# Kernel tuning notes

Hardware: AMD Instinct MI355X
Metric: run time of the kernel (lower is better)

Reference implementation:

```python
import jax, jax.numpy as jnp
import numpy as np

B, S, D, H = 2, 2048, 1024, 16
DH = D // H


def setup_inputs() -> dict:
    key = jax.random.key(0)
    ks = jax.random.split(key, 6)
    scale = 1.0 / np.sqrt(D)
    x = jax.random.normal(ks[0], (B, S, D), dtype=jnp.float32)
    mask = jnp.tril(jnp.ones((S, S), dtype=jnp.int32))  # causal 0/1 mask
    Wq = jax.random.normal(ks[1], (D, D), dtype=jnp.float32) * scale
    Wk = jax.random.normal(ks[2], (D, D), dtype=jnp.float32) * scale
    Wv = jax.random.normal(ks[3], (D, D), dtype=jnp.float32) * scale
    Wo = jax.random.normal(ks[4], (D, D), dtype=jnp.float32) * scale
    z = jnp.zeros((D,), dtype=jnp.float32)
    return {"x": x, "mask": mask, "Wq": Wq, "bq": z, "Wk": Wk, "bk": z,
            "Wv": Wv, "bv": z, "Wo": Wo, "bo": z}


def reference(x, mask, Wq, bq, Wk, bk, Wv, bv, Wo, bo):
    # Linear projections (torch Linear: x @ W.T + b; here W stored as [in, out])
    Q = x @ Wq + bq
    K = x @ Wk + bk
    V = x @ Wv + bv
    # [B, S, D] -> [B, H, S, DH]
    Q = Q.reshape(B, S, H, DH).transpose(0, 2, 1, 3)
    K = K.reshape(B, S, H, DH).transpose(0, 2, 1, 3)
    V = V.reshape(B, S, H, DH).transpose(0, 2, 1, 3)
    # scores: [B, H, S, S]
    attn = jnp.einsum('bhqd,bhkd->bhqk', Q, K) / jnp.sqrt(jnp.float32(DH))
    attn = jnp.where(mask == 0, jnp.float32(-1e9), attn)
    scores = jax.nn.softmax(attn, axis=-1)
    # dropout is identity in eval mode
    out = jnp.einsum('bhqk,bhkd->bhqd', scores, V)
    out = out.transpose(0, 2, 1, 3).reshape(B, S, D)
    return out @ Wo + bo
```

## Files before the change

kernel.cpp:

```cpp
#include <hip/hip_runtime.h>
#include <hip/hip_bf16.h>


typedef short bf16x8 __attribute__((ext_vector_type(8)));
typedef float f32x4  __attribute__((ext_vector_type(4)));
typedef short s16x4  __attribute__((ext_vector_type(4)));

#define BB 2
#define SS 2048
#define DD 1024
#define HH 16
#define DHH 64

__device__ __forceinline__ unsigned short f2bf(float f) {
    unsigned u = __builtin_bit_cast(unsigned, f);
    u += 0x7FFFu + ((u >> 16) & 1u);
    return (unsigned short)(u >> 16);
}
__device__ __forceinline__ unsigned short f2bf_trunc(float f) {
    return (unsigned short)(__builtin_bit_cast(unsigned, f) >> 16);
}
__device__ __forceinline__ void cp16(const unsigned short* g, unsigned short* l) {
    __builtin_amdgcn_global_load_lds(
        (const __attribute__((address_space(1))) unsigned int*)(g),
        (__attribute__((address_space(3))) unsigned int*)(l), 16, 0, 0);
}

__global__ __launch_bounds__(256) void prep(
    const float* __restrict__ x,
    const float* __restrict__ w0, const float* __restrict__ w1,
    const float* __restrict__ w2, const float* __restrict__ w3,
    unsigned short* __restrict__ xbf, unsigned short* __restrict__ wt) {
    __shared__ float tile[64][65];
    const int bid = blockIdx.x;
    const int tid = threadIdx.x;
    if (bid < 4096) {
        int i = (bid * 256 + tid) * 4;
        float4 v = *reinterpret_cast<const float4*>(x + i);
        s16x4 p;
        p[0] = (short)f2bf(v.x); p[1] = (short)f2bf(v.y);
        p[2] = (short)f2bf(v.z); p[3] = (short)f2bf(v.w);
        *reinterpret_cast<s16x4*>(xbf + i) = p;
        return;
    }
    const int tb = bid - 4096;
    const int z  = tb >> 8;
    const int bx = (tb & 15) * 64, by = ((tb >> 4) & 15) * 64;
    const float* src = z == 0 ? w0 : z == 1 ? w1 : z == 2 ? w2 : w3;
    unsigned short* out = wt + (size_t)z * (DD * DD);
    const int tx = tid & 63, ty = tid >> 6;
    #pragma unroll
    for (int i = 0; i < 64; i += 4)
        tile[ty + i][tx] = src[(size_t)(by + ty + i) * DD + bx + tx];
    __syncthreads();
    #pragma unroll
    for (int i = 0; i < 64; i += 4)
        out[(size_t)(bx + ty + i) * DD + by + tx] = f2bf(tile[tx][ty + i]);
}

__global__ __launch_bounds__(256) void gemm_qkv(
    const unsigned short* __restrict__ A, const unsigned short* __restrict__ Wt,
    const float* __restrict__ b0, const float* __restrict__ b1,
    const float* __restrict__ b2,
    unsigned short* __restrict__ d0, unsigned short* __restrict__ d1,
    unsigned short* __restrict__ d2) {
    __shared__ __align__(16) unsigned short As[128 * 64];
    __shared__ __align__(16) unsigned short Bs[128 * 64];

    const int tid  = threadIdx.x;
    const int lane = tid & 63;
    const int w    = tid >> 6;
    const int col  = lane & 15;
    const int quad = lane >> 4;
    const int wm   = (w >> 1) * 64;
    const int wn   = (w & 1) * 64;
    const int mb   = blockIdx.y * 128;
    const int nb   = blockIdx.x * 128;

    const int r8 = lane >> 3, gg = lane & 7;
    const int srcoff = ((gg ^ r8) * 8);
    const int cswz = col & 7;

    f32x4 acc[4][4];
    #pragma unroll
    for (int i = 0; i < 4; i++)
        #pragma unroll
        for (int j = 0; j < 4; j++) acc[i][j] = (f32x4){0.f, 0.f, 0.f, 0.f};

    for (int kt = 0; kt < 1024; kt += 64) {
        __syncthreads();
        #pragma unroll
        for (int it = 0; it < 4; it++) {
            int row = w * 32 + it * 8 + r8;
            cp16(A  + (size_t)(mb + row) * 1024 + kt + srcoff, As + (w * 32 + it * 8) * 64);
            cp16(Wt + (size_t)(nb + row) * 1024 + kt + srcoff, Bs + (w * 32 + it * 8) * 64);
        }
        __syncthreads();
        #pragma unroll
        for (int kk = 0; kk < 64; kk += 32) {
            const int kg = (kk >> 3) + quad;
            const int pos = ((kg ^ cswz) * 8);
            bf16x8 af[4], bfr[4];
            #pragma unroll
            for (int i = 0; i < 4; i++)
                af[i] = *reinterpret_cast<const bf16x8*>(As + (wm + i * 16 + col) * 64 + pos);
            #pragma unroll
            for (int j = 0; j < 4; j++)
                bfr[j] = *reinterpret_cast<const bf16x8*>(Bs + (wn + j * 16 + col) * 64 + pos);
            #pragma unroll
            for (int i = 0; i < 4; i++)
                #pragma unroll
                for (int j = 0; j < 4; j++)
                    acc[i][j] = __builtin_amdgcn_mfma_f32_16x16x32_bf16(af[i], bfr[j], acc[i][j], 0, 0, 0);
        }
    }

    const float QSCALE = 0.125f * 1.44269504f;
    #pragma unroll
    for (int i = 0; i < 4; i++) {
        int mg = mb + wm + i * 16 + quad * 4;
        #pragma unroll
        for (int j = 0; j < 4; j++) {
            int ng = nb + wn + j * 16 + col;
            int sel = ng >> 10, n2 = ng & 1023;
            int h = n2 >> 6, dd2 = n2 & 63;
            int b = mg >> 11, s = mg & 2047;
            int bh = b * HH + h;
            const float* bp = sel == 0 ? b0 : sel == 1 ? b1 : b2;
            float bbv = bp[n2];
            if (sel == 0) {
                #pragma unroll
                for (int r = 0; r < 4; r++)
                    d0[((size_t)bh * SS + s + r) * DHH + dd2] = f2bf((acc[i][j][r] + bbv) * QSCALE);
            } else if (sel == 1) {
                #pragma unroll
                for (int r = 0; r < 4; r++)
                    d1[((size_t)bh * SS + s + r) * DHH + dd2] = f2bf(acc[i][j][r] + bbv);
            } else {
                s16x4 pack;
                #pragma unroll
                for (int r = 0; r < 4; r++) pack[r] = (short)f2bf(acc[i][j][r] + bbv);
                *reinterpret_cast<s16x4*>(d2 + ((size_t)bh * DHH + dd2) * SS + s) = pack;
            }
        }
    }
}

__global__ __launch_bounds__(256) void gemm_out(
    const unsigned short* __restrict__ A, const unsigned short* __restrict__ Wt,
    const float* __restrict__ b0, float* __restrict__ d0f) {
    __shared__ __align__(16) unsigned short As[128 * 64];
    __shared__ __align__(16) unsigned short Bs[64 * 64];

    const int tid  = threadIdx.x;
    const int lane = tid & 63;
    const int w    = tid >> 6;
    const int col  = lane & 15;
    const int quad = lane >> 4;
    const int wm   = (w >> 1) * 64;
    const int wn   = (w & 1) * 32;
    const int mb   = blockIdx.y * 128;
    const int nb   = blockIdx.x * 64;

    const int r8 = lane >> 3, gg = lane & 7;
    const int srcoff = ((gg ^ r8) * 8);
    const int cswz = col & 7;

    f32x4 acc[4][2];
    #pragma unroll
    for (int i = 0; i < 4; i++)
        #pragma unroll
        for (int j = 0; j < 2; j++) acc[i][j] = (f32x4){0.f, 0.f, 0.f, 0.f};

    for (int kt = 0; kt < 1024; kt += 64) {
        __syncthreads();
        #pragma unroll
        for (int it = 0; it < 4; it++) {
            int row = w * 32 + it * 8 + r8;
            cp16(A + (size_t)(mb + row) * 1024 + kt + srcoff, As + (w * 32 + it * 8) * 64);
        }
        cp16(Wt + (size_t)(nb + w * 16 + r8) * 1024 + kt + srcoff, Bs + (w * 16) * 64);
        cp16(Wt + (size_t)(nb + w * 16 + 8 + r8) * 1024 + kt + srcoff, Bs + (w * 16 + 8) * 64);
        __syncthreads();
        #pragma unroll
        for (int kk = 0; kk < 64; kk += 32) {
            const int kg = (kk >> 3) + quad;
            const int pos = ((kg ^ cswz) * 8);
            bf16x8 af[4], bfr[2];
            #pragma unroll
            for (int i = 0; i < 4; i++)
                af[i] = *reinterpret_cast<const bf16x8*>(As + (wm + i * 16 + col) * 64 + pos);
            #pragma unroll
            for (int j = 0; j < 2; j++)
                bfr[j] = *reinterpret_cast<const bf16x8*>(Bs + (wn + j * 16 + col) * 64 + pos);
            #pragma unroll
            for (int i = 0; i < 4; i++)
                #pragma unroll
                for (int j = 0; j < 2; j++)
                    acc[i][j] = __builtin_amdgcn_mfma_f32_16x16x32_bf16(af[i], bfr[j], acc[i][j], 0, 0, 0);
        }
    }

    #pragma unroll
    for (int i = 0; i < 4; i++) {
        int mg = mb + wm + i * 16 + quad * 4;
        #pragma unroll
        for (int j = 0; j < 2; j++) {
            int ng = nb + wn + j * 16 + col;
            float bbv = b0[ng];
            #pragma unroll
            for (int r = 0; r < 4; r++)
                d0f[(size_t)(mg + r) * 1024 + ng] = acc[i][j][r] + bbv;
        }
    }
}

__global__ __launch_bounds__(256, 3) void attn(
    const unsigned short* __restrict__ Q, const unsigned short* __restrict__ K,
    const unsigned short* __restrict__ Vt, unsigned short* __restrict__ O) {
    __shared__ __align__(16) unsigned short Ks[2][64 * 64];
    __shared__ __align__(16) unsigned short Vs[2][64 * 64];
    __shared__ __align__(16) unsigned short Ps[4][16 * 72];

    const int tid  = threadIdx.x;
    const int lane = tid & 63;
    const int w    = tid >> 6;
    const int col  = lane & 15;
    const int quad = lane >> 4;
    const int bh   = blockIdx.x & 31;
    const int qt   = 31 - (blockIdx.x >> 5);
    const int qb   = qt * 64;
    const int r8 = lane >> 3, gg = lane & 7;
    const int srcoff = ((gg ^ r8) * 8);
    const int cswz = col & 7;
    const int pos0 = (quad       ^ cswz) * 8;
    const int pos1 = ((4 + quad) ^ cswz) * 8;

    bf16x8 onesf;
    #pragma unroll
    for (int j = 0; j < 8; j++) onesf[j] = (col == 0) ? (short)0x3F80 : (short)0;

    const int qrow = qb + w * 16 + col;
    const size_t qbase = ((size_t)bh * SS + qrow) * DHH;
    bf16x8 qlo = *reinterpret_cast<const bf16x8*>(Q + qbase + quad * 8);
    bf16x8 qhi = *reinterpret_cast<const bf16x8*>(Q + qbase + 32 + quad * 8);

    f32x4 o[5];
    #pragma unroll
    for (int d = 0; d < 5; d++) o[d] = (f32x4){0.f, 0.f, 0.f, 0.f};
    float m_i[4];
    #pragma unroll
    for (int r = 0; r < 4; r++) m_i[r] = -1e30f;

    const int ntiles = qt + 1;
    for (int t0 = 0; t0 < ntiles; t0 += 2) {
        const bool two = (t0 + 1 < ntiles);
        __syncthreads();
        #pragma unroll
        for (int it = 0; it < 2; it++) {
            int row = w * 16 + it * 8 + r8;
            cp16(K  + ((size_t)bh * SS + t0 * 64 + row) * DHH + srcoff,
                 Ks[0] + (w * 16 + it * 8) * 64);
            cp16(Vt + ((size_t)bh * DHH + row) * SS + t0 * 64 + srcoff,
                 Vs[0] + (w * 16 + it * 8) * 64);
        }
        if (two) {
            #pragma unroll
            for (int it = 0; it < 2; it++) {
                int row = w * 16 + it * 8 + r8;
                cp16(K  + ((size_t)bh * SS + (t0 + 1) * 64 + row) * DHH + srcoff,
                     Ks[1] + (w * 16 + it * 8) * 64);
                cp16(Vt + ((size_t)bh * DHH + row) * SS + (t0 + 1) * 64 + srcoff,
                     Vs[1] + (w * 16 + it * 8) * 64);
            }
        }
        __syncthreads();

        f32x4 sc[8];
        #pragma unroll
        for (int nt = 0; nt < 4; nt++) {
            int key = nt * 16 + col;
            bf16x8 klo = *reinterpret_cast<const bf16x8*>(Ks[0] + key * 64 + pos0);
            bf16x8 khi = *reinterpret_cast<const bf16x8*>(Ks[0] + key * 64 + pos1);
            f32x4 z = (f32x4){0.f, 0.f, 0.f, 0.f};
            z = __builtin_amdgcn_mfma_f32_16x16x32_bf16(qlo, klo, z, 0, 0, 0);
            z = __builtin_amdgcn_mfma_f32_16x16x32_bf16(qhi, khi, z, 0, 0, 0);
            sc[nt] = z;
        }
        if (two) {
            #pragma unroll
            for (int nt = 0; nt < 4; nt++) {
                int key = nt * 16 + col;
                bf16x8 klo = *reinterpret_cast<const bf16x8*>(Ks[1] + key * 64 + pos0);
                bf16x8 khi = *reinterpret_cast<const bf16x8*>(Ks[1] + key * 64 + pos1);
                f32x4 z = (f32x4){0.f, 0.f, 0.f, 0.f};
                z = __builtin_amdgcn_mfma_f32_16x16x32_bf16(qlo, klo, z, 0, 0, 0);
                z = __builtin_amdgcn_mfma_f32_16x16x32_bf16(qhi, khi, z, 0, 0, 0);
                sc[4 + nt] = z;
            }
        }
        if (t0 == qt || (two && t0 + 1 == qt)) {
            const int sb = (t0 == qt) ? 0 : 4;
            const int tb = (t0 == qt) ? t0 : t0 + 1;
            #pragma unroll
            for (int nt = 0; nt < 4; nt++) {
                int kg = tb * 64 + nt * 16 + col;
                #pragma unroll
                for (int r = 0; r < 4; r++) {
                    int qg = qb + w * 16 + quad * 4 + r;
                    if (kg > qg) sc[sb + nt][r] = -3.0e38f;
                }
            }
        }
        float mnew[4];
        bool upd = false;
        #pragma unroll
        for (int r = 0; r < 4; r++) {
            float t = fmaxf(fmaxf(sc[0][r], sc[1][r]), fmaxf(sc[2][r], sc[3][r]));
            if (two)
                t = fmaxf(t, fmaxf(fmaxf(sc[4][r], sc[5][r]), fmaxf(sc[6][r], sc[7][r])));
            t = fmaxf(t, __shfl_xor(t, 1));
            t = fmaxf(t, __shfl_xor(t, 2));
            t = fmaxf(t, __shfl_xor(t, 4));
            t = fmaxf(t, __shfl_xor(t, 8));
            mnew[r] = fmaxf(m_i[r], t);
            upd = upd || (mnew[r] > m_i[r]);
        }
        if (__any(upd)) {
            #pragma unroll
            for (int r = 0; r < 4; r++) {
                float a = exp2f(m_i[r] - mnew[r]);
                #pragma unroll
                for (int d = 0; d < 5; d++) o[d][r] *= a;
            }
        }
        #pragma unroll
        for (int r = 0; r < 4; r++) m_i[r] = mnew[r];

        unsigned short* pw = Ps[w];
        #pragma unroll
        for (int nt = 0; nt < 4; nt++)
            #pragma unroll
            for (int r = 0; r < 4; r++)
                pw[(quad * 4 + r) * 72 + nt * 16 + col] = f2bf_trunc(exp2f(sc[nt][r] - mnew[r]));
        {
            bf16x8 pf0 = *reinterpret_cast<const bf16x8*>(pw + col * 72 + quad * 8);
            bf16x8 pf1 = *reinterpret_cast<const bf16x8*>(pw + col * 72 + 32 + quad * 8);
            #pragma unroll
            for (int dt = 0; dt < 4; dt++) {
                int rv = dt * 16 + col;
                bf16x8 vf0 = *reinterpret_cast<const bf16x8*>(Vs[0] + rv * 64 + pos0);
                bf16x8 vf1 = *reinterpret_cast<const bf16x8*>(Vs[0] + rv * 64 + pos1);
                o[dt] = __builtin_amdgcn_mfma_f32_16x16x32_bf16(pf0, vf0, o[dt], 0, 0, 0);
                o[dt] = __builtin_amdgcn_mfma_f32_16x16x32_bf16(pf1, vf1, o[dt], 0, 0, 0);
            }
            o[4] = __builtin_amdgcn_mfma_f32_16x16x32_bf16(pf0, onesf, o[4], 0, 0, 0);
            o[4] = __builtin_amdgcn_mfma_f32_16x16x32_bf16(pf1, onesf, o[4], 0, 0, 0);
        }
        if (two) {
            #pragma unroll
            for (int nt = 0; nt < 4; nt++)
                #pragma unroll
                for (int r = 0; r < 4; r++)
                    pw[(quad * 4 + r) * 72 + nt * 16 + col] = f2bf_trunc(exp2f(sc[4 + nt][r] - mnew[r]));
            bf16x8 pf0 = *reinterpret_cast<const bf16x8*>(pw + col * 72 + quad * 8);
            bf16x8 pf1 = *reinterpret_cast<const bf16x8*>(pw + col * 72 + 32 + quad * 8);
            #pragma unroll
            for (int dt = 0; dt < 4; dt++) {
                int rv = dt * 16 + col;
                bf16x8 vf0 = *reinterpret_cast<const bf16x8*>(Vs[1] + rv * 64 + pos0);
                bf16x8 vf1 = *reinterpret_cast<const bf16x8*>(Vs[1] + rv * 64 + pos1);
                o[dt] = __builtin_amdgcn_mfma_f32_16x16x32_bf16(pf0, vf0, o[dt], 0, 0, 0);
                o[dt] = __builtin_amdgcn_mfma_f32_16x16x32_bf16(pf1, vf1, o[dt], 0, 0, 0);
            }
            o[4] = __builtin_amdgcn_mfma_f32_16x16x32_bf16(pf0, onesf, o[4], 0, 0, 0);
            o[4] = __builtin_amdgcn_mfma_f32_16x16x32_bf16(pf1, onesf, o[4], 0, 0, 0);
        }
    }

    #pragma unroll
    for (int r = 0; r < 4; r++) {
        float lv = __shfl(o[4][r], lane & 48);
        float inv = 1.0f / lv;
        int sq = qb + w * 16 + quad * 4 + r;
        size_t base = ((size_t)(bh >> 4) * SS + sq) * DD + (size_t)(bh & 15) * DHH;
        #pragma unroll
        for (int dt = 0; dt < 4; dt++)
            O[base + dt * 16 + col] = f2bf(o[dt][r] * inv);
    }
}

extern "C" void kernel_launch(void* const* d_in, const int* in_sizes, int n_in,
                              void* d_out, int out_size, void* d_ws, size_t ws_size,
                              hipStream_t stream) {
    (void)in_sizes; (void)n_in; (void)out_size; (void)ws_size;
    const float* x  = (const float*)d_in[0];
    const float* Wq = (const float*)d_in[2];
    const float* bq = (const float*)d_in[3];
    const float* Wk = (const float*)d_in[4];
    const float* bk = (const float*)d_in[5];
    const float* Wv = (const float*)d_in[6];
    const float* bv = (const float*)d_in[7];
    const float* Wo = (const float*)d_in[8];
    const float* bo = (const float*)d_in[9];
    float* out = (float*)d_out;

    char* ws = (char*)d_ws;
    unsigned short* xbf = (unsigned short*)(ws);
    unsigned short* qws = (unsigned short*)(ws + ((size_t)8  << 20));
    unsigned short* kws = (unsigned short*)(ws + ((size_t)16 << 20));
    unsigned short* vws = (unsigned short*)(ws + ((size_t)24 << 20));
    unsigned short* wt  = (unsigned short*)(ws + ((size_t)32 << 20));
    unsigned short* ows = xbf;

    prep<<<dim3(5120), 256, 0, stream>>>(x, Wq, Wk, Wv, Wo, xbf, wt);
    gemm_qkv<<<dim3(24, 32), 256, 0, stream>>>(xbf, wt, bq, bk, bv,
                                               qws, kws, vws);
    attn<<<dim3(1024), 256, 0, stream>>>(qws, kws, vws, ows);
    gemm_out<<<dim3(16, 32), 256, 0, stream>>>(ows, wt + (size_t)3 * 1024 * 1024,
                                               bo, out);
}
```

Before: 211.5 us.

## Compute transposed scores so P stays in registers, dropping LDS round-trip

The QK^T MFMA operands are swapped so each lane holds scores for a single query row across keys. K rows are loaded into LDS in a permuted order so the register layout of the probabilities matches the A-operand layout the PV MFMA expects. This removes the per-wave P staging buffer in shared memory and its store/load round-trip. The row max now needs only two cross-lane shuffles, and the rescale factor is fetched per row with a shuffle. Launch bounds are raised to 5 blocks per CU to use the freed LDS and registers, at the risk of register pressure or spills.

```diff
diff --git a/kernel.cpp b/kernel.cpp
--- a/kernel.cpp
+++ b/kernel.cpp
@@ -215,12 +215,11 @@
     }
 }
 
-__global__ __launch_bounds__(256, 3) void attn(
+__global__ __launch_bounds__(256, 5) void attn(
     const unsigned short* __restrict__ Q, const unsigned short* __restrict__ K,
     const unsigned short* __restrict__ Vt, unsigned short* __restrict__ O) {
     __shared__ __align__(16) unsigned short Ks[2][64 * 64];
     __shared__ __align__(16) unsigned short Vs[2][64 * 64];
-    __shared__ __align__(16) unsigned short Ps[4][16 * 72];
 
     const int tid  = threadIdx.x;
     const int lane = tid & 63;
@@ -248,9 +247,7 @@
     f32x4 o[5];
     #pragma unroll
     for (int d = 0; d < 5; d++) o[d] = (f32x4){0.f, 0.f, 0.f, 0.f};
-    float m_i[4];
-    #pragma unroll
-    for (int r = 0; r < 4; r++) m_i[r] = -1e30f;
+    float m_i = -1e30f;
 
     const int ntiles = qt + 1;
     for (int t0 = 0; t0 < ntiles; t0 += 2) {
@@ -258,20 +255,22 @@
         __syncthreads();
         #pragma unroll
         for (int it = 0; it < 2; it++) {
-            int row = w * 16 + it * 8 + r8;
-            cp16(K  + ((size_t)bh * SS + t0 * 64 + row) * DHH + srcoff,
-                 Ks[0] + (w * 16 + it * 8) * 64);
-            cp16(Vt + ((size_t)bh * DHH + row) * SS + t0 * 64 + srcoff,
-                 Vs[0] + (w * 16 + it * 8) * 64);
+            int drow = w * 16 + it * 8;
+            int skey = (w >> 1) * 32 + it * 16 + (r8 >> 2) * 8 + (w & 1) * 4 + (r8 & 3);
+            cp16(K  + ((size_t)bh * SS + t0 * 64 + skey) * DHH + srcoff,
+                 Ks[0] + drow * 64);
+            cp16(Vt + ((size_t)bh * DHH + drow + r8) * SS + t0 * 64 + srcoff,
+                 Vs[0] + drow * 64);
         }
         if (two) {
             #pragma unroll
             for (int it = 0; it < 2; it++) {
-                int row = w * 16 + it * 8 + r8;
-                cp16(K  + ((size_t)bh * SS + (t0 + 1) * 64 + row) * DHH + srcoff,
-                     Ks[1] + (w * 16 + it * 8) * 64);
-                cp16(Vt + ((size_t)bh * DHH + row) * SS + (t0 + 1) * 64 + srcoff,
-                     Vs[1] + (w * 16 + it * 8) * 64);
+                int drow = w * 16 + it * 8;
+                int skey = (w >> 1) * 32 + it * 16 + (r8 >> 2) * 8 + (w & 1) * 4 + (r8 & 3);
+                cp16(K  + ((size_t)bh * SS + (t0 + 1) * 64 + skey) * DHH + srcoff,
+                     Ks[1] + drow * 64);
+                cp16(Vt + ((size_t)bh * DHH + drow + r8) * SS + (t0 + 1) * 64 + srcoff,
+                     Vs[1] + drow * 64);
             }
         }
         __syncthreads();
@@ -279,23 +278,23 @@
         f32x4 sc[8];
         #pragma unroll
         for (int nt = 0; nt < 4; nt++) {
-            int key = nt * 16 + col;
-            bf16x8 klo = *reinterpret_cast<const bf16x8*>(Ks[0] + key * 64 + pos0);
-            bf16x8 khi = *reinterpret_cast<const bf16x8*>(Ks[0] + key * 64 + pos1);
+            int krow = nt * 16 + col;
+            bf16x8 klo = *reinterpret_cast<const bf16x8*>(Ks[0] + krow * 64 + pos0);
+            bf16x8 khi = *reinterpret_cast<const bf16x8*>(Ks[0] + krow * 64 + pos1);
             f32x4 z = (f32x4){0.f, 0.f, 0.f, 0.f};
-            z = __builtin_amdgcn_mfma_f32_16x16x32_bf16(qlo, klo, z, 0, 0, 0);
-            z = __builtin_amdgcn_mfma_f32_16x16x32_bf16(qhi, khi, z, 0, 0, 0);
+            z = __builtin_amdgcn_mfma_f32_16x16x32_bf16(klo, qlo, z, 0, 0, 0);
+            z = __builtin_amdgcn_mfma_f32_16x16x32_bf16(khi, qhi, z, 0, 0, 0);
             sc[nt] = z;
         }
         if (two) {
             #pragma unroll
             for (int nt = 0; nt < 4; nt++) {
-                int key = nt * 16 + col;
-                bf16x8 klo = *reinterpret_cast<const bf16x8*>(Ks[1] + key * 64 + pos0);
-                bf16x8 khi = *reinterpret_cast<const bf16x8*>(Ks[1] + key * 64 + pos1);
+                int krow = nt * 16 + col;
+                bf16x8 klo = *reinterpret_cast<const bf16x8*>(Ks[1] + krow * 64 + pos0);
+                bf16x8 khi = *reinterpret_cast<const bf16x8*>(Ks[1] + krow * 64 + pos1);
                 f32x4 z = (f32x4){0.f, 0.f, 0.f, 0.f};
-                z = __builtin_amdgcn_mfma_f32_16x16x32_bf16(qlo, klo, z, 0, 0, 0);
-                z = __builtin_amdgcn_mfma_f32_16x16x32_bf16(qhi, khi, z, 0, 0, 0);
+                z = __builtin_amdgcn_mfma_f32_16x16x32_bf16(klo, qlo, z, 0, 0, 0);
+                z = __builtin_amdgcn_mfma_f32_16x16x32_bf16(khi, qhi, z, 0, 0, 0);
                 sc[4 + nt] = z;
             }
         }
@@ -304,48 +303,44 @@
             const int tb = (t0 == qt) ? t0 : t0 + 1;
             #pragma unroll
             for (int nt = 0; nt < 4; nt++) {
-                int kg = tb * 64 + nt * 16 + col;
                 #pragma unroll
                 for (int r = 0; r < 4; r++) {
-                    int qg = qb + w * 16 + quad * 4 + r;
-                    if (kg > qg) sc[sb + nt][r] = -3.0e38f;
+                    int kg = tb * 64 + (nt >> 1) * 32 + quad * 8 + (nt & 1) * 4 + r;
+                    if (kg > qrow) sc[sb + nt][r] = -3.0e38f;
                 }
             }
         }
-        float mnew[4];
-        bool upd = false;
-        #pragma unroll
-        for (int r = 0; r < 4; r++) {
-            float t = fmaxf(fmaxf(sc[0][r], sc[1][r]), fmaxf(sc[2][r], sc[3][r]));
-            if (two)
-                t = fmaxf(t, fmaxf(fmaxf(sc[4][r], sc[5][r]), fmaxf(sc[6][r], sc[7][r])));
-            t = fmaxf(t, __shfl_xor(t, 1));
-            t = fmaxf(t, __shfl_xor(t, 2));
-            t = fmaxf(t, __shfl_xor(t, 4));
-            t = fmaxf(t, __shfl_xor(t, 8));
-            mnew[r] = fmaxf(m_i[r], t);
-            upd = upd || (mnew[r] > m_i[r]);
-        }
+        float mx = fmaxf(fmaxf(sc[0][0], sc[0][1]), fmaxf(sc[0][2], sc[0][3]));
+        #pragma unroll
+        for (int nt = 1; nt < 4; nt++)
+            mx = fmaxf(mx, fmaxf(fmaxf(sc[nt][0], sc[nt][1]), fmaxf(sc[nt][2], sc[nt][3])));
+        if (two) {
+            #pragma unroll
+            for (int nt = 4; nt < 8; nt++)
+                mx = fmaxf(mx, fmaxf(fmaxf(sc[nt][0], sc[nt][1]), fmaxf(sc[nt][2], sc[nt][3])));
+        }
+        mx = fmaxf(mx, __shfl_xor(mx, 16));
+        mx = fmaxf(mx, __shfl_xor(mx, 32));
+        float mnew = fmaxf(m_i, mx);
+        bool upd = (mnew > m_i);
         if (__any(upd)) {
+            float delta = m_i - mnew;
             #pragma unroll
             for (int r = 0; r < 4; r++) {
-                float a = exp2f(m_i[r] - mnew[r]);
+                float a = exp2f(__shfl(delta, quad * 4 + r));
                 #pragma unroll
                 for (int d = 0; d < 5; d++) o[d][r] *= a;
             }
         }
-        #pragma unroll
-        for (int r = 0; r < 4; r++) m_i[r] = mnew[r];
-
-        unsigned short* pw = Ps[w];
-        #pragma unroll
-        for (int nt = 0; nt < 4; nt++)
-            #pragma unroll
-            for (int r = 0; r < 4; r++)
-                pw[(quad * 4 + r) * 72 + nt * 16 + col] = f2bf_trunc(exp2f(sc[nt][r] - mnew[r]));
+        m_i = mnew;
+
         {
-            bf16x8 pf0 = *reinterpret_cast<const bf16x8*>(pw + col * 72 + quad * 8);
-            bf16x8 pf1 = *reinterpret_cast<const bf16x8*>(pw + col * 72 + 32 + quad * 8);
+            bf16x8 pf0, pf1;
+            #pragma unroll
+            for (int j = 0; j < 8; j++) {
+                pf0[j] = (short)f2bf_trunc(exp2f(sc[(j >> 2)][j & 3] - mnew));
+                pf1[j] = (short)f2bf_trunc(exp2f(sc[2 + (j >> 2)][j & 3] - mnew));
+            }
             #pragma unroll
             for (int dt = 0; dt < 4; dt++) {
                 int rv = dt * 16 + col;
@@ -358,13 +353,12 @@
             o[4] = __builtin_amdgcn_mfma_f32_16x16x32_bf16(pf1, onesf, o[4], 0, 0, 0);
         }
         if (two) {
-            #pragma unroll
-            for (int nt = 0; nt < 4; nt++)
-                #pragma unroll
-                for (int r = 0; r < 4; r++)
-                    pw[(quad * 4 + r) * 72 + nt * 16 + col] = f2bf_trunc(exp2f(sc[4 + nt][r] - mnew[r]));
-            bf16x8 pf0 = *reinterpret_cast<const bf16x8*>(pw + col * 72 + quad * 8);
-            bf16x8 pf1 = *reinterpret_cast<const bf16x8*>(pw + col * 72 + 32 + quad * 8);
+            bf16x8 pf0, pf1;
+            #pragma unroll
+            for (int j = 0; j < 8; j++) {
+                pf0[j] = (short)f2bf_trunc(exp2f(sc[4 + (j >> 2)][j & 3] - mnew));
+                pf1[j] = (short)f2bf_trunc(exp2f(sc[6 + (j >> 2)][j & 3] - mnew));
+            }
             #pragma unroll
             for (int dt = 0; dt < 4; dt++) {
                 int rv = dt * 16 + col;
```

After: 261.4 us. 23.6% more time.
